# Kernel optimization log

Hardware: AMD Instinct MI355X
Metric: run time of the kernel (lower is better)

Reference implementation:

```python
import jax, jax.numpy as jnp
import numpy as np

N_EMBED = 1024
N_HEAD = 16
HEAD_DIM = N_EMBED // N_HEAD
N_CONTEXT = 2048
MASKED_BIAS = -10000.0


def setup_inputs() -> dict:
    key = jax.random.key(0)
    k1, k2, k3 = jax.random.split(key, 3)
    hidden_states = jax.random.normal(k1, (4, 2048, N_EMBED), dtype=jnp.float32)
    w_attn = jax.random.normal(k2, (N_EMBED, 3 * N_EMBED), dtype=jnp.float32) * 0.02
    b_attn = jnp.zeros((3 * N_EMBED,), dtype=jnp.float32)
    w_proj = jax.random.normal(k3, (N_EMBED, N_EMBED), dtype=jnp.float32) * 0.02
    b_proj = jnp.zeros((N_EMBED,), dtype=jnp.float32)
    return {"hidden_states": hidden_states, "w_attn": w_attn, "b_attn": b_attn,
            "w_proj": w_proj, "b_proj": b_proj}


def reference(hidden_states, w_attn, b_attn, w_proj, b_proj):
    B, S, E = hidden_states.shape
    # c_attn: Conv1D (x @ W + b)
    qkv = hidden_states @ w_attn + b_attn  # [B,S,3E]
    q, k, v = jnp.split(qkv, 3, axis=-1)
    # split heads -> [B,H,S,D]
    def split_heads(x):
        return x.reshape(B, S, N_HEAD, HEAD_DIM).transpose(0, 2, 1, 3)
    q = split_heads(q)
    k = split_heads(k)  # torch permutes key to [B,H,D,S]; we keep [B,H,S,D] and einsum
    v = split_heads(v)
    # attention scores scaled by sqrt(head_dim) (v.size(-1) == HEAD_DIM)
    w = jnp.einsum('bhqd,bhkd->bhqk', q, k) / jnp.float32(HEAD_DIM) ** 0.5
    causal = jnp.tril(jnp.ones((S, S), dtype=bool))  # bias buffer slice
    w = jnp.where(causal[None, None], w, jnp.asarray(MASKED_BIAS, w.dtype))
    w = jax.nn.softmax(w, axis=-1)  # dropout p=0 -> identity
    out = jnp.einsum('bhqk,bhkd->bhqd', w, v)  # [B,H,S,D]
    # merge heads
    out = out.transpose(0, 2, 1, 3).reshape(B, S, E)
    out = out @ w_proj + b_proj
    # key returned in torch layout [B,H,D,S]
    return out, k.transpose(0, 1, 3, 2), v
```

## Files before the change

### kernel.cpp

```cpp
#include <hip/hip_runtime.h>
#include <hip/hip_bf16.h>


typedef __attribute__((ext_vector_type(8))) short bfx8;
typedef __attribute__((ext_vector_type(4))) short bfx4;
typedef __attribute__((ext_vector_type(4))) float fx4;

#define MFMA(a, b, c) __builtin_amdgcn_mfma_f32_16x16x32_bf16(a, b, c, 0, 0, 0)

#define S_CTX 2048
#define NE 1024
#define NH 16
#define HD 64

#define QSCALE 0.18033688011112042f

__device__ __forceinline__ short f2bf(float f) {
  unsigned u = __float_as_uint(f);
  unsigned r = u + 0x7fffu + ((u >> 16) & 1u);
  return (short)(r >> 16);
}

__device__ __forceinline__ unsigned pkbf(float a, float b) {
  union {
    __hip_bfloat162 h;
    unsigned u;
  } c;
  c.h = __float22bfloat162_rn(make_float2(a, b));
  return c.u;
}

__device__ __forceinline__ void gload16(const void* g, void* l) {
  __builtin_amdgcn_global_load_lds(
      (const __attribute__((address_space(1))) unsigned int*)g,
      (__attribute__((address_space(3))) unsigned int*)l, 16, 0, 0);
}

__global__ __launch_bounds__(256) void convert_bf16_kernel(const float* __restrict__ in,
                                                           short* __restrict__ out) {
  size_t i = (size_t)blockIdx.x * 256 + threadIdx.x;
  fx4 v = *(const fx4*)(in + i * 4);
  bfx4 o;
#pragma unroll
  for (int j = 0; j < 4; ++j) o[j] = f2bf(v[j]);
  *(bfx4*)(out + i * 4) = o;
}

__global__ __launch_bounds__(256) void transpose_conv_kernel(const float* __restrict__ in,
                                                             short* __restrict__ out,
                                                             int R, int C) {
  __shared__ float tile[32][33];
  int tx = threadIdx.x, ty = threadIdx.y;
  int c0 = blockIdx.x * 32, r0 = blockIdx.y * 32;
#pragma unroll
  for (int i = 0; i < 4; ++i)
    tile[ty + i * 8][tx] = in[(size_t)(r0 + ty + i * 8) * C + c0 + tx];
  __syncthreads();
#pragma unroll
  for (int i = 0; i < 4; ++i)
    out[(size_t)(c0 + ty + i * 8) * R + r0 + tx] = f2bf(tile[tx][ty + i * 8]);
}

__device__ __forceinline__ void gemm128_mainloop(const short* __restrict__ A,
                                                 const short* __restrict__ B,
                                                 const int K, const int m0, const int n0,
                                                 short* As, short* Bs, fx4 acc[4][4]) {
  const int t = threadIdx.x;
  const int lane = t & 63, w = t >> 6;
  const int g = lane >> 4, li = lane & 15;
  const int wr = w >> 1, wc = w & 1;
  const int bsw = ((lane & 7) ^ (lane >> 3)) * 8;
  const int rowl = w * 8 + (lane >> 3);

  for (int k0 = 0; k0 < K; k0 += 64) {
#pragma unroll
    for (int i = 0; i < 4; ++i) {
      const int row = i * 32 + rowl;
      gload16(A + (size_t)(m0 + row) * K + k0 + bsw, (char*)As + i * 4096 + w * 1024);
      gload16(B + (size_t)(n0 + row) * K + k0 + bsw, (char*)Bs + i * 4096 + w * 1024);
    }
    __syncthreads();
#pragma unroll
    for (int ks = 0; ks < 2; ++ks) {
      bfx8 af[4], bf[4];
#pragma unroll
      for (int m = 0; m < 4; ++m) {
        const int R = wr * 64 + m * 16 + li;
        af[m] = *(const bfx8*)((const char*)As + R * 128 + (((ks * 4 + g) ^ (li & 7)) << 4));
      }
#pragma unroll
      for (int n = 0; n < 4; ++n) {
        const int R = wc * 64 + n * 16 + li;
        bf[n] = *(const bfx8*)((const char*)Bs + R * 128 + (((ks * 4 + g) ^ (li & 7)) << 4));
      }
#pragma unroll
      for (int m = 0; m < 4; ++m)
#pragma unroll
        for (int n = 0; n < 4; ++n)
          acc[m][n] = MFMA(af[m], bf[n], acc[m][n]);
    }
    __syncthreads();
  }
}

__global__ __launch_bounds__(256) void gemm_qkv_kernel(const short* __restrict__ X,
                                                       const short* __restrict__ WT,
                                                       const float* __restrict__ bias,
                                                       short* __restrict__ qbf,
                                                       short* __restrict__ kbf,
                                                       short* __restrict__ vT,
                                                       float* __restrict__ kT,
                                                       float* __restrict__ vout) {
  __shared__ short As[128 * 64];
  __shared__ short Bs[128 * 64];
  fx4 acc[4][4];
  const fx4 z = {0.f, 0.f, 0.f, 0.f};
#pragma unroll
  for (int m = 0; m < 4; ++m)
#pragma unroll
    for (int n = 0; n < 4; ++n) acc[m][n] = z;
  const int m0 = blockIdx.y * 128, n0 = blockIdx.x * 128;
  gemm128_mainloop(X, WT, 1024, m0, n0, As, Bs, acc);

  const int lane = threadIdx.x & 63, w = threadIdx.x >> 6;
  const int g = lane >> 4, li = lane & 15;
  const int wr = w >> 1, wc = w & 1;
  const int sec = n0 >> 10;
#pragma unroll
  for (int mf = 0; mf < 4; ++mf) {
#pragma unroll
    for (int nf = 0; nf < 4; ++nf) {
      const int mrow = m0 + wr * 64 + mf * 16 + g * 4;
      const int ncol = n0 + wc * 64 + nf * 16 + li;
      const float bv = bias[ncol];
      fx4 vv;
#pragma unroll
      for (int jj = 0; jj < 4; ++jj) vv[jj] = acc[mf][nf][jj] + bv;
      const int b = mrow >> 11, s = mrow & 2047;
      const int e = ncol & 1023, h = e >> 6, d = e & 63;
      const size_t bidx = ((size_t)((b * 16 + h) * 2048 + s)) * 64 + d;
      if (sec == 0) {
#pragma unroll
        for (int jj = 0; jj < 4; ++jj) qbf[bidx + (size_t)jj * 64] = f2bf(vv[jj] * QSCALE);
      } else if (sec == 1) {
#pragma unroll
        for (int jj = 0; jj < 4; ++jj) kbf[bidx + (size_t)jj * 64] = f2bf(vv[jj]);
        const size_t tb = ((size_t)((b * 16 + h) * 64 + d)) * 2048 + s;
        *(fx4*)(kT + tb) = vv;
      } else {
#pragma unroll
        for (int jj = 0; jj < 4; ++jj) vout[bidx + (size_t)jj * 64] = vv[jj];
        const size_t tb = ((size_t)((b * 16 + h) * 64 + d)) * 2048 + s;
        bfx4 pv;
#pragma unroll
        for (int jj = 0; jj < 4; ++jj) pv[jj] = f2bf(vv[jj]);
        *(bfx4*)(vT + tb) = pv;
      }
    }
  }
}

__global__ __launch_bounds__(256) void gemm_proj_kernel(const short* __restrict__ X,
                                                        const short* __restrict__ WT,
                                                        const float* __restrict__ bias,
                                                        float* __restrict__ out) {
  __shared__ short As[128 * 64];
  __shared__ short Bs[128 * 64];
  fx4 acc[4][4];
  const fx4 z = {0.f, 0.f, 0.f, 0.f};
#pragma unroll
  for (int m = 0; m < 4; ++m)
#pragma unroll
    for (int n = 0; n < 4; ++n) acc[m][n] = z;
  const int m0 = blockIdx.y * 128, n0 = blockIdx.x * 128;
  gemm128_mainloop(X, WT, 1024, m0, n0, As, Bs, acc);

  const int lane = threadIdx.x & 63, w = threadIdx.x >> 6;
  const int g = lane >> 4, li = lane & 15;
  const int wr = w >> 1, wc = w & 1;
#pragma unroll
  for (int mf = 0; mf < 4; ++mf) {
#pragma unroll
    for (int nf = 0; nf < 4; ++nf) {
      const int mrow = m0 + wr * 64 + mf * 16 + g * 4;
      const int ncol = n0 + wc * 64 + nf * 16 + li;
      const float bv = bias[ncol];
#pragma unroll
      for (int jj = 0; jj < 4; ++jj)
        out[(size_t)(mrow + jj) * 1024 + ncol] = acc[mf][nf][jj] + bv;
    }
  }
}

#define KSW(base, row, byte) ((char*)(base) + (row) * 128 + ((byte) ^ (((row) & 7) << 4)))

#define SOFTMAX_TILE(stv, accv, mrun, lrun, pAv, qm, diag)                    \
  {                                                                          \
    if (diag) {                                                              \
      const int qg = (qm) + li;                                              \
      _Pragma("unroll") for (int kt = 0; kt < 4; ++kt)                       \
          _Pragma("unroll") for (int jj = 0; jj < 4; ++jj) if (              \
              k0 + kt * 16 + g * 4 + jj > qg) stv[kt][jj] = -1e30f;          \
    }                                                                        \
    float pm = stv[0][0];                                                    \
    _Pragma("unroll") for (int kt = 0; kt < 4; ++kt)                         \
        _Pragma("unroll") for (int jj = 0; jj < 4; ++jj) pm =                \
            fmaxf(pm, stv[kt][jj]);                                          \
    if (!__all(pm <= (mrun) + 6.0f)) {                                       \
      pm = fmaxf(pm, __shfl_xor(pm, 16));                                    \
      pm = fmaxf(pm, __shfl_xor(pm, 32));                                    \
      const float mn = fmaxf((mrun), pm);                                    \
      const float rf = __builtin_amdgcn_exp2f((mrun) - mn);                  \
      (lrun) *= rf;                                                          \
      fx4 rfv;                                                               \
      _Pragma("unroll") for (int jj = 0; jj < 4; ++jj) rfv[jj] =             \
          __shfl(rf, g * 4 + jj);                                            \
      _Pragma("unroll") for (int dt = 0; dt < 4; ++dt) accv[dt] *= rfv;      \
      (mrun) = mn;                                                           \
    }                                                                        \
    union {                                                                  \
      bfx8 v;                                                                \
      unsigned u[4];                                                         \
    } pk_[2];                                                                \
    float ls = 0.f;                                                          \
    _Pragma("unroll") for (int kt = 0; kt < 4; ++kt) {                       \
      const float p0 = __builtin_amdgcn_exp2f(stv[kt][0] - (mrun));          \
      const float p1 = __builtin_amdgcn_exp2f(stv[kt][1] - (mrun));          \
      const float p2 = __builtin_amdgcn_exp2f(stv[kt][2] - (mrun));          \
      const float p3 = __builtin_amdgcn_exp2f(stv[kt][3] - (mrun));          \
      ls += (p0 + p1) + (p2 + p3);                                           \
      pk_[kt >> 1].u[(kt & 1) * 2 + 0] = pkbf(p0, p1);                       \
      pk_[kt >> 1].u[(kt & 1) * 2 + 1] = pkbf(p2, p3);                       \
    }                                                                        \
    ls += __shfl_xor(ls, 16);                                                \
    ls += __shfl_xor(ls, 32);                                                \
    (lrun) += ls;                                                            \
    pAv[0] = pk_[0].v;                                                       \
    pAv[1] = pk_[1].v;                                                       \
  }

__global__ __launch_bounds__(256, 4) void attn_kernel(const short* __restrict__ Q,
                                                      const short* __restrict__ Kc,
                                                      const short* __restrict__ VT,
                                                      short* __restrict__ O) {
  __shared__ short Ks[2][64 * 64];
  __shared__ short Vs[2][64 * 64];

  const int bh = blockIdx.x & 63;
  const int c = blockIdx.x >> 6;

  const int t = threadIdx.x;
  const int w = t >> 6;
  const int lane = t & 63;
  const int g = lane >> 4, li = lane & 15;

  const size_t hoff = (size_t)bh * (S_CTX * HD);
  const short* Qh = Q + hoff;
  const char* Khc = (const char*)(Kc + hoff);
  const char* Vhc = (const char*)(VT + hoff);

  const int lr = lane >> 3;
  const int bsw = ((lane & 7) ^ lr) * 16;
  const int rb0 = w * 16;

  const int qm0 = 64 * c + 16 * w;
  const int qm1 = 64 * (31 - c) + 16 * w;
  bfx8 qf0[2], qf1[2];
  qf0[0] = *(const bfx8*)(Qh + (size_t)(qm0 + li) * HD + g * 8);
  qf0[1] = *(const bfx8*)(Qh + (size_t)(qm0 + li) * HD + 32 + g * 8);
  qf1[0] = *(const bfx8*)(Qh + (size_t)(qm1 + li) * HD + g * 8);
  qf1[1] = *(const bfx8*)(Qh + (size_t)(qm1 + li) * HD + 32 + g * 8);

  fx4 acc0[4], acc1[4];
  const fx4 z = {0.f, 0.f, 0.f, 0.f};
#pragma unroll
  for (int dt = 0; dt < 4; ++dt) {
    acc0[dt] = z;
    acc1[dt] = z;
  }
  float m0 = -1e30f, l0 = 0.f, m1 = -1e30f, l1 = 0.f;

  const int tmax = 31 - c;

#define STAGE_TILE(k0s, buf)                                                        \
  {                                                                                 \
    _Pragma("unroll") for (int i = 0; i < 2; ++i) {                                 \
      const int rb = rb0 + i * 8;                                                   \
      const int row = rb + lr;                                                      \
      gload16(Khc + (size_t)((k0s) + row) * 128 + bsw, (char*)Ks[buf] + rb * 128);  \
      gload16(Vhc + (size_t)row * (S_CTX * 2) + (size_t)(k0s) * 2 + bsw,            \
              (char*)Vs[buf] + rb * 128);                                           \
    }                                                                               \
  }

  STAGE_TILE(0, 0);
  __syncthreads();

  for (int tt = 0; tt <= tmax; ++tt) {
    const int cur = tt & 1;
    const int k0 = tt * 64;
    if (tt < tmax) STAGE_TILE(k0 + 64, cur ^ 1);
    const bool act0 = (tt <= c);

    bfx8 pA0[2], pA1[2];
    {
      fx4 st[4] = {z, z, z, z};
#pragma unroll
      for (int h = 0; h < 2; ++h) {
        bfx8 kfh[4];
#pragma unroll
        for (int kt = 0; kt < 4; ++kt)
          kfh[kt] = *(const bfx8*)KSW(Ks[cur], kt * 16 + li, h * 64 + g * 16);
#pragma unroll
        for (int kt = 0; kt < 4; ++kt) st[kt] = MFMA(kfh[kt], qf1[h], st[kt]);
      }
      SOFTMAX_TILE(st, acc1, m1, l1, pA1, qm1, tt == tmax);
    }
    if (act0) {
      fx4 st[4] = {z, z, z, z};
#pragma unroll
      for (int h = 0; h < 2; ++h) {
        bfx8 kfh[4];
#pragma unroll
        for (int kt = 0; kt < 4; ++kt)
          kfh[kt] = *(const bfx8*)KSW(Ks[cur], kt * 16 + li, h * 64 + g * 16);
#pragma unroll
        for (int kt = 0; kt < 4; ++kt) st[kt] = MFMA(kfh[kt], qf0[h], st[kt]);
      }
      SOFTMAX_TILE(st, acc0, m0, l0, pA0, qm0, tt == c);
    }
#pragma unroll
    for (int kc = 0; kc < 2; ++kc) {
      bfx8 vfc[4];
#pragma unroll
      for (int dt = 0; dt < 4; ++dt) {
        const int row = dt * 16 + li;
        const bfx4 a = *(const bfx4*)KSW(Vs[cur], row, kc * 64 + g * 8);
        const bfx4 b = *(const bfx4*)KSW(Vs[cur], row, kc * 64 + 32 + g * 8);
        bfx8 vv;
#pragma unroll
        for (int j = 0; j < 4; ++j) {
          vv[j] = a[j];
          vv[j + 4] = b[j];
        }
        vfc[dt] = vv;
      }
#pragma unroll
      for (int dt = 0; dt < 4; ++dt) acc1[dt] = MFMA(pA1[kc], vfc[dt], acc1[dt]);
      if (act0) {
#pragma unroll
        for (int dt = 0; dt < 4; ++dt) acc0[dt] = MFMA(pA0[kc], vfc[dt], acc0[dt]);
      }
    }
    __syncthreads();
  }

  const int b = bh >> 4, h = bh & 15;
#pragma unroll
  for (int mf = 0; mf < 2; ++mf) {
    const int qm = mf ? qm1 : qm0;
    const float lr_ = mf ? l1 : l0;
    fx4 lv;
#pragma unroll
    for (int jj = 0; jj < 4; ++jj)
      lv[jj] = __builtin_amdgcn_rcpf(__shfl(lr_, g * 4 + jj));
#pragma unroll
    for (int dt = 0; dt < 4; ++dt)
#pragma unroll
      for (int jj = 0; jj < 4; ++jj) {
        const int s = qm + g * 4 + jj;
        const fx4 av = mf ? acc1[dt] : acc0[dt];
        O[((size_t)(b * S_CTX + s)) * NE + h * HD + dt * 16 + li] =
            f2bf(av[jj] * lv[jj]);
      }
  }
}

extern "C" void kernel_launch(void* const* d_in, const int* in_sizes, int n_in,
                              void* d_out, int out_size, void* d_ws, size_t ws_size,
                              hipStream_t stream) {
  const float* hs = (const float*)d_in[0];
  const float* w_attn = (const float*)d_in[1];
  const float* b_attn = (const float*)d_in[2];
  const float* w_proj = (const float*)d_in[3];
  const float* b_proj = (const float*)d_in[4];

  float* out = (float*)d_out;
  float* kT_out = out + 8388608;
  float* v_out = out + 2 * 8388608;

  char* ws = (char*)d_ws;
  short* xbf = (short*)ws;
  short* waT = (short*)(ws + 16777216);
  short* vTb = (short*)(ws + 23068672);
  short* qbf = (short*)(ws + 39845888);
  short* kbf = (short*)(ws + 56623104);
  short* wpT = (short*)(ws + 73400320);

  convert_bf16_kernel<<<8192, 256, 0, stream>>>(hs, xbf);
  transpose_conv_kernel<<<dim3(96, 32), dim3(32, 8), 0, stream>>>(w_attn, waT, 1024, 3072);
  transpose_conv_kernel<<<dim3(32, 32), dim3(32, 8), 0, stream>>>(w_proj, wpT, 1024, 1024);
  gemm_qkv_kernel<<<dim3(24, 64), 256, 0, stream>>>(xbf, waT, b_attn, qbf, kbf, vTb,
                                                    kT_out, v_out);
  attn_kernel<<<1024, 256, 0, stream>>>(qbf, kbf, vTb, xbf );
  gemm_proj_kernel<<<dim3(8, 64), 256, 0, stream>>>(xbf, wpT, b_proj, out);
}
```

Measured before the change: 183.7 us.

## Double-buffer LDS tiles in GEMM mainloop and swap grid axes for reuse

The GEMM mainloop now ping-pongs between two LDS buffers, issuing global loads for the next K-tile before computing on the current one, and synchronizes once per iteration instead of twice. The QKV and projection launches swap grid dimensions so adjacent blocks share the same weight column tile, improving cache reuse. LDS use per block doubles, which may reduce occupancy.

```diff
diff --git a/kernel.cpp b/kernel.cpp
--- a/kernel.cpp
+++ b/kernel.cpp
@@ -72,26 +72,38 @@
   const int bsw = ((lane & 7) ^ (lane >> 3)) * 8;
   const int rowl = w * 8 + (lane >> 3);
 
-  for (int k0 = 0; k0 < K; k0 += 64) {
-#pragma unroll
-    for (int i = 0; i < 4; ++i) {
-      const int row = i * 32 + rowl;
-      gload16(A + (size_t)(m0 + row) * K + k0 + bsw, (char*)As + i * 4096 + w * 1024);
-      gload16(B + (size_t)(n0 + row) * K + k0 + bsw, (char*)Bs + i * 4096 + w * 1024);
-    }
-    __syncthreads();
+#define GSTAGE(k0s, buf)                                                   \
+  {                                                                        \
+    _Pragma("unroll") for (int i = 0; i < 4; ++i) {                        \
+      const int row = i * 32 + rowl;                                       \
+      gload16(A + (size_t)(m0 + row) * K + (k0s) + bsw,                    \
+              (char*)As + (buf) * 16384 + i * 4096 + w * 1024);            \
+      gload16(B + (size_t)(n0 + row) * K + (k0s) + bsw,                    \
+              (char*)Bs + (buf) * 16384 + i * 4096 + w * 1024);            \
+    }                                                                      \
+  }
+
+  GSTAGE(0, 0);
+  __syncthreads();
+
+  const int nt = K >> 6;
+  for (int tt = 0; tt < nt; ++tt) {
+    const int cur = tt & 1;
+    if (tt + 1 < nt) GSTAGE((tt + 1) * 64, cur ^ 1);
+    const char* Ab = (const char*)As + cur * 16384;
+    const char* Bb = (const char*)Bs + cur * 16384;
 #pragma unroll
     for (int ks = 0; ks < 2; ++ks) {
       bfx8 af[4], bf[4];
 #pragma unroll
       for (int m = 0; m < 4; ++m) {
         const int R = wr * 64 + m * 16 + li;
-        af[m] = *(const bfx8*)((const char*)As + R * 128 + (((ks * 4 + g) ^ (li & 7)) << 4));
+        af[m] = *(const bfx8*)(Ab + R * 128 + (((ks * 4 + g) ^ (li & 7)) << 4));
       }
 #pragma unroll
       for (int n = 0; n < 4; ++n) {
         const int R = wc * 64 + n * 16 + li;
-        bf[n] = *(const bfx8*)((const char*)Bs + R * 128 + (((ks * 4 + g) ^ (li & 7)) << 4));
+        bf[n] = *(const bfx8*)(Bb + R * 128 + (((ks * 4 + g) ^ (li & 7)) << 4));
       }
 #pragma unroll
       for (int m = 0; m < 4; ++m)
@@ -101,6 +113,7 @@
     }
     __syncthreads();
   }
+#undef GSTAGE
 }
 
 __global__ __launch_bounds__(256) void gemm_qkv_kernel(const short* __restrict__ X,
@@ -111,15 +124,15 @@
                                                        short* __restrict__ vT,
                                                        float* __restrict__ kT,
                                                        float* __restrict__ vout) {
-  __shared__ short As[128 * 64];
-  __shared__ short Bs[128 * 64];
+  __shared__ short As[2 * 128 * 64];
+  __shared__ short Bs[2 * 128 * 64];
   fx4 acc[4][4];
   const fx4 z = {0.f, 0.f, 0.f, 0.f};
 #pragma unroll
   for (int m = 0; m < 4; ++m)
 #pragma unroll
     for (int n = 0; n < 4; ++n) acc[m][n] = z;
-  const int m0 = blockIdx.y * 128, n0 = blockIdx.x * 128;
+  const int m0 = blockIdx.x * 128, n0 = blockIdx.y * 128;
   gemm128_mainloop(X, WT, 1024, m0, n0, As, Bs, acc);
 
   const int lane = threadIdx.x & 63, w = threadIdx.x >> 6;
@@ -164,15 +177,15 @@
                                                         const short* __restrict__ WT,
                                                         const float* __restrict__ bias,
                                                         float* __restrict__ out) {
-  __shared__ short As[128 * 64];
-  __shared__ short Bs[128 * 64];
+  __shared__ short As[2 * 128 * 64];
+  __shared__ short Bs[2 * 128 * 64];
   fx4 acc[4][4];
   const fx4 z = {0.f, 0.f, 0.f, 0.f};
 #pragma unroll
   for (int m = 0; m < 4; ++m)
 #pragma unroll
     for (int n = 0; n < 4; ++n) acc[m][n] = z;
-  const int m0 = blockIdx.y * 128, n0 = blockIdx.x * 128;
+  const int m0 = blockIdx.x * 128, n0 = blockIdx.y * 128;
   gemm128_mainloop(X, WT, 1024, m0, n0, As, Bs, acc);
 
   const int lane = threadIdx.x & 63, w = threadIdx.x >> 6;
@@ -400,8 +413,8 @@
   convert_bf16_kernel<<<8192, 256, 0, stream>>>(hs, xbf);
   transpose_conv_kernel<<<dim3(96, 32), dim3(32, 8), 0, stream>>>(w_attn, waT, 1024, 3072);
   transpose_conv_kernel<<<dim3(32, 32), dim3(32, 8), 0, stream>>>(w_proj, wpT, 1024, 1024);
-  gemm_qkv_kernel<<<dim3(24, 64), 256, 0, stream>>>(xbf, waT, b_attn, qbf, kbf, vTb,
+  gemm_qkv_kernel<<<dim3(64, 24), 256, 0, stream>>>(xbf, waT, b_attn, qbf, kbf, vTb,
                                                     kT_out, v_out);
   attn_kernel<<<1024, 256, 0, stream>>>(qbf, kbf, vTb, xbf );
-  gemm_proj_kernel<<<dim3(8, 64), 256, 0, stream>>>(xbf, wpT, b_proj, out);
-}
+  gemm_proj_kernel<<<dim3(64, 8), 256, 0, stream>>>(xbf, wpT, b_proj, out);
+}
```

Measured after the change: 192.2 us. 1.05x slower.
